# Kernel tuning notes

Hardware: AMD Instinct MI355X
Metric: run time of the kernel (lower is better)

## Reference

```python
import jax, jax.numpy as jnp
from jax import lax
import numpy as np

# correlation hyperparams (from init_kwargs)
MAX_D = 32      # maxDisplacement
PAD = 1         # zero padding
K = 3           # patch (kernel) size
STRIDE_K = 1    # stride over output pixels
STRIDE_D = 1    # stride over displacements


def setup_inputs() -> dict:
    key = jax.random.key(0)
    k0, k1 = jax.random.split(key)
    x0 = jax.random.normal(k0, (4, 64, 256, 512), dtype=jnp.float32)
    x1 = jax.random.normal(k1, (4, 64, 256, 512), dtype=jnp.float32)
    return {"x0": x0, "x1": x1}


def _corr2d(x0, x1):
    # x0, x1: [B, C, H, W] NCHW feature maps
    B, C, H, W = x0.shape
    # zero-pad spatially; x1 gets extra width padding so all displacements are in-bounds
    x0p = jnp.pad(x0, ((0, 0), (0, 0), (PAD, PAD), (PAD, PAD)))
    x1p = jnp.pad(x1, ((0, 0), (0, 0), (PAD, PAD), (PAD + MAX_D, PAD + MAX_D)))
    Wp = W + 2 * PAD
    # width offsets into x1p for displacements d = -MAX_D .. MAX_D step STRIDE_D
    offsets = jnp.arange(0, 2 * MAX_D + 1, STRIDE_D, dtype=jnp.int32)

    def step(carry, off):
        x1s = lax.dynamic_slice_in_dim(x1p, off, Wp, axis=3)   # [B,C,Hp,Wp]
        prod = jnp.sum(x0p * x1s, axis=1)                      # channel dot -> [B,Hp,Wp]
        # KxK box-sum over the patch, stride STRIDE_K -> [B,Ho,Wo]
        s = lax.reduce_window(prod, jnp.float32(0), lax.add,
                              (1, K, K), (1, STRIDE_K, STRIDE_K), 'VALID')
        return carry, s

    _, out = lax.scan(step, None, offsets)        # [nD, B, Ho, Wo]
    out = jnp.transpose(out, (1, 0, 2, 3))        # [B, nD, Ho, Wo]
    return out / jnp.asarray(K * K * C, out.dtype)


def reference(x0, x1):
    return _corr2d(x0, x1)
```

## Files before the change

kernel.cpp:

```cpp
#include <hip/hip_runtime.h>

#define WF 512
#define HF 256
#define CF 64
#define NDTOT 65
#define DP 72

static constexpr size_t CH  = (size_t)HF * WF;
static constexpr size_t WH  = (size_t)HF * WF;
static constexpr float  INV = 1.0f / 576.0f;

typedef _Float16 f16;
typedef _Float16 f16x8 __attribute__((ext_vector_type(8)));
typedef float    f32x4 __attribute__((ext_vector_type(4)));

typedef __attribute__((address_space(3))) void lds_void_t;
typedef const __attribute__((address_space(1))) void glb_void_t;

__global__ __launch_bounds__(256, 4)
void corr_gram(const float* __restrict__ x0, const float* __restrict__ x1,
               f16* __restrict__ ws) {
    const int f = blockIdx.x;
    const int xcd = f & 7;
    const int strip = (f >> 3) & 3;
    const int pl = f >> 5;
    const int pair = xcd * 128 + pl;
    const int y = pair & 255;
    const int b = pair >> 8;

    const int t = threadIdx.x;
    const int l = t & 63;
    const int w = t >> 6;
    const int xs = strip << 7;
    const int jb = xs - 32;

    const int n   = l & 15;
    const int n4  = n >> 2, nr = n & 3;
    const int ksl = (l >> 4) * 8;
    const int qs  = ((l >> 4) & 3) << 2;

    __shared__ float lds[10240];

    const float* x0r = x0 + (size_t)b * CF * CH + (size_t)y * WF;
    const float* x1r = x1 + (size_t)b * CF * CH + (size_t)y * WF;

    int o0[4], o1[6];
#pragma unroll
    for (int qi = 0; qi < 4; ++qi) {
        const int P = qi * 256 + t;
        const int L = P ^ (((P >> 8) & 3) << 2);
        o0[qi] = (L >> 5) * (int)CH + xs + 4 * (L & 31);
    }
#pragma unroll
    for (int ri = 0; ri < 6; ++ri) {
        const int P = ri * 256 + t;
        const int c = P / 48;
        const int j4 = (P - 48 * c) ^ (((c >> 3) & 3) << 2);
        int jg = jb + 4 * j4;
        jg = jg < 0 ? 0 : (jg > 508 ? 508 : jg);
        o1[ri] = c * (int)CH + jg;
    }

    const int A0b = (ksl * 32 + ((8 * w + n4) ^ qs)) * 4 + nr;
    const int A1b = (ksl * 32 + ((8 * w + 4 + n4) ^ qs)) * 4 + nr;
    int Bb[6];
#pragma unroll
    for (int jt = 0; jt < 6; ++jt)
        Bb[jt] = 4096 + (48 * ksl + ((8 * w + 4 * jt + n4) ^ qs)) * 4 + nr;

    f32x4 acc[10];
#pragma unroll
    for (int i = 0; i < 10; ++i) acc[i] = (f32x4)0.0f;

#define TRIPLE(ai, AH, AL) \
    do { \
        acc[ai] = __builtin_amdgcn_mfma_f32_16x16x32_f16(AH, bh, acc[ai], 0, 0, 0); \
        acc[ai] = __builtin_amdgcn_mfma_f32_16x16x32_f16(AH, bl, acc[ai], 0, 0, 0); \
        acc[ai] = __builtin_amdgcn_mfma_f32_16x16x32_f16(AL, bh, acc[ai], 0, 0, 0); \
    } while (0)

#pragma unroll
    for (int h = 0; h < 2; ++h) {
        const size_t hb = (size_t)h * 32 * CH;
#pragma unroll
        for (int qi = 0; qi < 4; ++qi)
            __builtin_amdgcn_global_load_lds(
                (glb_void_t*)(x0r + hb + o0[qi]),
                (lds_void_t*)(lds + (qi * 256 + w * 64) * 4), 16, 0, 0);
#pragma unroll
        for (int ri = 0; ri < 6; ++ri)
            __builtin_amdgcn_global_load_lds(
                (glb_void_t*)(x1r + hb + o1[ri]),
                (lds_void_t*)(lds + 4096 + (ri * 256 + w * 64) * 4), 16, 0, 0);

        __syncthreads();

        f16x8 ah0, al0, ah1, al1;
        {
            float ar[8];
#pragma unroll
            for (int i = 0; i < 8; ++i) ar[i] = lds[A0b + i * 128];
#pragma unroll
            for (int i = 0; i < 8; ++i) {
                const f16 hv = (f16)ar[i];
                ah0[i] = hv; al0[i] = (f16)(ar[i] - (float)hv);
            }
#pragma unroll
            for (int i = 0; i < 8; ++i) ar[i] = lds[A1b + i * 128];
#pragma unroll
            for (int i = 0; i < 8; ++i) {
                const f16 hv = (f16)ar[i];
                ah1[i] = hv; al1[i] = (f16)(ar[i] - (float)hv);
            }
        }

#pragma unroll
        for (int jt = 0; jt < 6; ++jt) {
            float br[8];
#pragma unroll
            for (int i = 0; i < 8; ++i) br[i] = lds[Bb[jt] + i * 192];
            const bool okB = (unsigned)(jb + (2 * w + jt) * 16 + n) < (unsigned)WF;
            f16x8 bh, bl;
#pragma unroll
            for (int i = 0; i < 8; ++i) {
                const float v = okB ? br[i] : 0.f;
                const f16 hv = (f16)v;
                bh[i] = hv; bl[i] = (f16)(v - (float)hv);
            }
            if (jt < 5) TRIPLE(jt, ah0, al0);
            if (jt >= 1) TRIPLE(4 + jt, ah1, al1);
        }

        __syncthreads();
    }
#undef TRIPLE

    f16* eb = (f16*)lds;

#pragma unroll
    for (int xtl = 0; xtl < 2; ++xtl) {
#pragma unroll
        for (int p = 0; p < 5; ++p) {
            const int i = xtl * 5 + p;
#pragma unroll
            for (int q = 0; q < 4; ++q) {
                const int m = (l >> 4) * 4 + q;
                const int xl = (2 * w + xtl) * 16 + m;
                const int d = 16 * p + n - m;
                if ((unsigned)d < (unsigned)NDTOT)
                    eb[xl * DP + d] = (f16)acc[i][q];
            }
        }
    }
#pragma unroll
    for (int i = 0; i < 4; ++i) {
        const int idx = t + 256 * i;
        if (idx < 896) {
            const int xl = idx / 7;
            eb[xl * DP + NDTOT + (idx - 7 * xl)] = (f16)0.f;
        }
    }
    __syncthreads();

    uint4* dst = (uint4*)(ws + ((size_t)(b * HF + y) * WF + xs) * DP);
    const uint4* src = (const uint4*)eb;
#pragma unroll
    for (int i = 0; i < 5; ++i) {
        const int idx = t + 256 * i;
        if (idx < 1152) dst[idx] = src[idx];
    }
}

__global__ __launch_bounds__(256)
void corr_box(const f16* __restrict__ ws, float* __restrict__ out) {
    const int xt = blockIdx.x;
    const int yt = blockIdx.y;
    const int b = blockIdx.z;
    const int t = threadIdx.x;
    const int x0b = xt * 32, y0 = yt * 8;

    __shared__ f16 S[10 * 34][DP];

    for (int u = 0; u < 10; ++u) {
        const int yy = y0 - 1 + u;
        const bool yok = (unsigned)yy < (unsigned)HF;
        const f16* src = ws + ((size_t)(b * HF + yy) * WF + (x0b - 1)) * DP;
#pragma unroll
        for (int sub = 0; sub < 2; ++sub) {
            const int idx = sub * 256 + t;
            if (idx < 306) {
                const int v = idx / 9, dg = idx - v * 9;
                const int xx = x0b - 1 + v;
                f16x8 val;
#pragma unroll
                for (int jj = 0; jj < 8; ++jj) val[jj] = (f16)0.f;
                if (yok && (unsigned)xx < (unsigned)WF)
                    val = *(const f16x8*)(src + (size_t)v * DP + dg * 8);
                *(f16x8*)&S[u * 34 + v][dg * 8] = val;
            }
        }
    }
    __syncthreads();

    const int ly = t >> 5, lx = t & 31;
    const int yg = y0 + ly, xg = x0b + lx;
    float* o0 = out + (size_t)b * NDTOT * WH + (size_t)yg * WF + xg;

#pragma unroll 1
    for (int dg = 0; dg < 9; ++dg) {
        f16x8 s;
#pragma unroll
        for (int jj = 0; jj < 8; ++jj) s[jj] = (f16)0.f;
#pragma unroll
        for (int du = 0; du < 3; ++du)
#pragma unroll
            for (int dv = 0; dv < 3; ++dv)
                s += *(const f16x8*)&S[(ly + du) * 34 + (lx + dv)][dg * 8];
#pragma unroll
        for (int jj = 0; jj < 8; ++jj) {
            const int d = dg * 8 + jj;
            if (d < NDTOT) o0[(size_t)d * WH] = (float)s[jj] * INV;
        }
    }
}

__global__ void corr_naive(const float* __restrict__ x0, const float* __restrict__ x1,
                           float* __restrict__ out) {
    const size_t total = (size_t)4 * NDTOT * WH;
    size_t idx = (size_t)blockIdx.x * blockDim.x + threadIdx.x;
    if (idx >= total) return;
    const int j = (int)(idx % WF);
    const int i = (int)((idx / WF) % HF);
    const int d = (int)((idx / WH) % NDTOT);
    const int b = (int)(idx / ((size_t)NDTOT * WH));
    const int disp = d - 32;
    float s = 0.f;
    for (int u = i - 1; u <= i + 1; ++u) {
        if (u < 0 || u >= HF) continue;
        for (int v = j - 1; v <= j + 1; ++v) {
            if (v < 0 || v >= WF) continue;
            const int v1c = v + disp;
            if (v1c < 0 || v1c >= WF) continue;
            const float* p0 = x0 + (size_t)b * CF * CH + (size_t)u * WF + v;
            const float* p1 = x1 + (size_t)b * CF * CH + (size_t)u * WF + v1c;
            for (int c = 0; c < CF; ++c)
                s += p0[(size_t)c * CH] * p1[(size_t)c * CH];
        }
    }
    out[idx] = s * INV;
}

extern "C" void kernel_launch(void* const* d_in, const int* in_sizes, int n_in,
                              void* d_out, int out_size, void* d_ws, size_t ws_size,
                              hipStream_t stream) {
    const float* x0 = (const float*)d_in[0];
    const float* x1 = (const float*)d_in[1];
    float* out = (float*)d_out;

    const size_t wsNeed = (size_t)4 * HF * WF * DP * sizeof(f16);

    if (ws_size >= wsNeed) {
        f16* ws = (f16*)d_ws;
        corr_gram<<<dim3(4096), dim3(256), 0, stream>>>(x0, x1, ws);
        corr_box<<<dim3(16, 32, 4), dim3(256), 0, stream>>>(ws, out);
    } else {
        const size_t total = (size_t)4 * NDTOT * WH;
        const int blocks = (int)((total + 255) / 256);
        corr_naive<<<dim3(blocks), dim3(256), 0, stream>>>(x0, x1, out);
    }
}
```

Before: 128.3 us.

## Make gram kernel persistent per row with double-buffered async LDS loads

The gram kernel now runs one block per (batch,row) and loops over the four x-strips and both channel halves as eight stages. Global-to-LDS loads are double-buffered and issued two stages ahead, with explicit vmcnt waits and barriers, so memory latency overlaps MFMA work. LDS doubles to 80KB and occupancy drops to two blocks per CU. The XCD-aware block remapping is removed and the grid shrinks from 4096 to 1024 blocks.

```diff
diff --git a/kernel.cpp b/kernel.cpp
--- a/kernel.cpp
+++ b/kernel.cpp
@@ -17,48 +17,48 @@
 typedef __attribute__((address_space(3))) void lds_void_t;
 typedef const __attribute__((address_space(1))) void glb_void_t;
 
-__global__ __launch_bounds__(256, 4)
+#define WAIT_VM10() asm volatile("s_waitcnt vmcnt(10)" ::: "memory")
+#define WAIT_VM0()  asm volatile("s_waitcnt vmcnt(0)" ::: "memory")
+#define WAIT_LGKM() asm volatile("s_waitcnt lgkmcnt(0)" ::: "memory")
+#define BAR()       __builtin_amdgcn_s_barrier()
+#define SFENCE()    __builtin_amdgcn_sched_barrier(0)
+
+__global__ __launch_bounds__(256, 2)
 void corr_gram(const float* __restrict__ x0, const float* __restrict__ x1,
                f16* __restrict__ ws) {
-    const int f = blockIdx.x;
-    const int xcd = f & 7;
-    const int strip = (f >> 3) & 3;
-    const int pl = f >> 5;
-    const int pair = xcd * 128 + pl;
-    const int y = pair & 255;
-    const int b = pair >> 8;
+    const int blk = blockIdx.x;
+    const int y = blk & 255;
+    const int b = blk >> 8;
 
     const int t = threadIdx.x;
     const int l = t & 63;
     const int w = t >> 6;
-    const int xs = strip << 7;
-    const int jb = xs - 32;
 
     const int n   = l & 15;
     const int n4  = n >> 2, nr = n & 3;
     const int ksl = (l >> 4) * 8;
     const int qs  = ((l >> 4) & 3) << 2;
 
-    __shared__ float lds[10240];
+    __shared__ float lds_flat[20480];
 
     const float* x0r = x0 + (size_t)b * CF * CH + (size_t)y * WF;
     const float* x1r = x1 + (size_t)b * CF * CH + (size_t)y * WF;
 
-    int o0[4], o1[6];
+    int o0c[4];
 #pragma unroll
     for (int qi = 0; qi < 4; ++qi) {
         const int P = qi * 256 + t;
         const int L = P ^ (((P >> 8) & 3) << 2);
-        o0[qi] = (L >> 5) * (int)CH + xs + 4 * (L & 31);
-    }
+        o0c[qi] = (L >> 5) * (int)CH + 4 * (L & 31);
+    }
+    int oc1[6], jo[6];
 #pragma unroll
     for (int ri = 0; ri < 6; ++ri) {
         const int P = ri * 256 + t;
         const int c = P / 48;
         const int j4 = (P - 48 * c) ^ (((c >> 3) & 3) << 2);
-        int jg = jb + 4 * j4;
-        jg = jg < 0 ? 0 : (jg > 508 ? 508 : jg);
-        o1[ri] = c * (int)CH + jg;
+        oc1[ri] = c * (int)CH;
+        jo[ri] = 4 * j4;
     }
 
     const int A0b = (ksl * 32 + ((8 * w + n4) ^ qs)) * 4 + nr;
@@ -68,9 +68,26 @@
     for (int jt = 0; jt < 6; ++jt)
         Bb[jt] = 4096 + (48 * ksl + ((8 * w + 4 * jt + n4) ^ qs)) * 4 + nr;
 
-    f32x4 acc[10];
-#pragma unroll
-    for (int i = 0; i < 10; ++i) acc[i] = (f32x4)0.0f;
+    auto issue_stage = [&](int s2) {
+        const int st2 = s2 >> 1, hf2 = s2 & 1;
+        const int xs2 = st2 << 7, jb2 = xs2 - 32;
+        float* dstb = lds_flat + (s2 & 1) * 10240;
+        const float* g0 = x0r + (size_t)(hf2 * 32) * CH;
+        const float* g1 = x1r + (size_t)(hf2 * 32) * CH;
+#pragma unroll
+        for (int qi = 0; qi < 4; ++qi)
+            __builtin_amdgcn_global_load_lds(
+                (glb_void_t*)(g0 + o0c[qi] + xs2),
+                (lds_void_t*)(dstb + (qi * 256 + w * 64) * 4), 16, 0, 0);
+#pragma unroll
+        for (int ri = 0; ri < 6; ++ri) {
+            int jg = jb2 + jo[ri];
+            jg = jg < 0 ? 0 : (jg > 508 ? 508 : jg);
+            __builtin_amdgcn_global_load_lds(
+                (glb_void_t*)(g1 + oc1[ri] + jg),
+                (lds_void_t*)(dstb + 4096 + (ri * 256 + w * 64) * 4), 16, 0, 0);
+        }
+    };
 
 #define TRIPLE(ai, AH, AL) \
     do { \
@@ -79,34 +96,40 @@
         acc[ai] = __builtin_amdgcn_mfma_f32_16x16x32_f16(AL, bh, acc[ai], 0, 0, 0); \
     } while (0)
 
-#pragma unroll
-    for (int h = 0; h < 2; ++h) {
-        const size_t hb = (size_t)h * 32 * CH;
-#pragma unroll
-        for (int qi = 0; qi < 4; ++qi)
-            __builtin_amdgcn_global_load_lds(
-                (glb_void_t*)(x0r + hb + o0[qi]),
-                (lds_void_t*)(lds + (qi * 256 + w * 64) * 4), 16, 0, 0);
-#pragma unroll
-        for (int ri = 0; ri < 6; ++ri)
-            __builtin_amdgcn_global_load_lds(
-                (glb_void_t*)(x1r + hb + o1[ri]),
-                (lds_void_t*)(lds + 4096 + (ri * 256 + w * 64) * 4), 16, 0, 0);
-
-        __syncthreads();
+    f32x4 acc[10];
+
+    issue_stage(0);
+    issue_stage(1);
+
+#pragma unroll 1
+    for (int s = 0; s < 8; ++s) {
+        const int st = s >> 1;
+        const int xs = st << 7, jb = xs - 32;
+        const float* bufc = lds_flat + (s & 1) * 10240;
+
+        if (s & 1) {
+        } else {
+#pragma unroll
+            for (int i = 0; i < 10; ++i) acc[i] = (f32x4)0.0f;
+        }
+
+        if (s < 7) WAIT_VM10(); else WAIT_VM0();
+        SFENCE();
+        BAR();
+        SFENCE();
 
         f16x8 ah0, al0, ah1, al1;
         {
             float ar[8];
 #pragma unroll
-            for (int i = 0; i < 8; ++i) ar[i] = lds[A0b + i * 128];
+            for (int i = 0; i < 8; ++i) ar[i] = bufc[A0b + i * 128];
 #pragma unroll
             for (int i = 0; i < 8; ++i) {
                 const f16 hv = (f16)ar[i];
                 ah0[i] = hv; al0[i] = (f16)(ar[i] - (float)hv);
             }
 #pragma unroll
-            for (int i = 0; i < 8; ++i) ar[i] = lds[A1b + i * 128];
+            for (int i = 0; i < 8; ++i) ar[i] = bufc[A1b + i * 128];
 #pragma unroll
             for (int i = 0; i < 8; ++i) {
                 const f16 hv = (f16)ar[i];
@@ -118,7 +141,7 @@
         for (int jt = 0; jt < 6; ++jt) {
             float br[8];
 #pragma unroll
-            for (int i = 0; i < 8; ++i) br[i] = lds[Bb[jt] + i * 192];
+            for (int i = 0; i < 8; ++i) br[i] = bufc[Bb[jt] + i * 192];
             const bool okB = (unsigned)(jb + (2 * w + jt) * 16 + n) < (unsigned)WF;
             f16x8 bh, bl;
 #pragma unroll
@@ -131,44 +154,56 @@
             if (jt >= 1) TRIPLE(4 + jt, ah1, al1);
         }
 
-        __syncthreads();
+        if (s & 1) {
+            WAIT_LGKM();
+            BAR();
+            SFENCE();
+            f16* eb = (f16*)bufc;
+#pragma unroll
+            for (int xtl = 0; xtl < 2; ++xtl) {
+#pragma unroll
+                for (int p = 0; p < 5; ++p) {
+                    const int i = xtl * 5 + p;
+#pragma unroll
+                    for (int q = 0; q < 4; ++q) {
+                        const int m = (l >> 4) * 4 + q;
+                        const int xl = (2 * w + xtl) * 16 + m;
+                        const int d = 16 * p + n - m;
+                        if ((unsigned)d < (unsigned)NDTOT)
+                            eb[xl * DP + d] = (f16)acc[i][q];
+                    }
+                }
+            }
+#pragma unroll
+            for (int i = 0; i < 4; ++i) {
+                const int idx = t + 256 * i;
+                if (idx < 896) {
+                    const int xl = idx / 7;
+                    eb[xl * DP + NDTOT + (idx - 7 * xl)] = (f16)0.f;
+                }
+            }
+            WAIT_LGKM();
+            BAR();
+            SFENCE();
+            uint4* dst = (uint4*)(ws + ((size_t)(b * HF + y) * WF + xs) * DP);
+            const uint4* src = (const uint4*)eb;
+#pragma unroll
+            for (int i = 0; i < 5; ++i) {
+                const int idx = t + 256 * i;
+                if (idx < 1152) dst[idx] = src[idx];
+            }
+            WAIT_LGKM();
+            BAR();
+            SFENCE();
+            if (s + 2 < 8) issue_stage(s + 2);
+        } else {
+            WAIT_LGKM();
+            BAR();
+            SFENCE();
+            if (s + 2 < 8) issue_stage(s + 2);
+        }
     }
 #undef TRIPLE
-
-    f16* eb = (f16*)lds;
-
-#pragma unroll
-    for (int xtl = 0; xtl < 2; ++xtl) {
-#pragma unroll
-        for (int p = 0; p < 5; ++p) {
-            const int i = xtl * 5 + p;
-#pragma unroll
-            for (int q = 0; q < 4; ++q) {
-                const int m = (l >> 4) * 4 + q;
-                const int xl = (2 * w + xtl) * 16 + m;
-                const int d = 16 * p + n - m;
-                if ((unsigned)d < (unsigned)NDTOT)
-                    eb[xl * DP + d] = (f16)acc[i][q];
-            }
-        }
-    }
-#pragma unroll
-    for (int i = 0; i < 4; ++i) {
-        const int idx = t + 256 * i;
-        if (idx < 896) {
-            const int xl = idx / 7;
-            eb[xl * DP + NDTOT + (idx - 7 * xl)] = (f16)0.f;
-        }
-    }
-    __syncthreads();
-
-    uint4* dst = (uint4*)(ws + ((size_t)(b * HF + y) * WF + xs) * DP);
-    const uint4* src = (const uint4*)eb;
-#pragma unroll
-    for (int i = 0; i < 5; ++i) {
-        const int idx = t + 256 * i;
-        if (idx < 1152) dst[idx] = src[idx];
-    }
 }
 
 __global__ __launch_bounds__(256)
@@ -261,7 +296,7 @@
 
     if (ws_size >= wsNeed) {
         f16* ws = (f16*)d_ws;
-        corr_gram<<<dim3(4096), dim3(256), 0, stream>>>(x0, x1, ws);
+        corr_gram<<<dim3(1024), dim3(256), 0, stream>>>(x0, x1, ws);
         corr_box<<<dim3(16, 32, 4), dim3(256), 0, stream>>>(ws, out);
     } else {
         const size_t total = (size_t)4 * NDTOT * WH;
```

Result: no change. 128.1 us (-0.1%).
